# Kernel tuning notes

Measured on AMD Instinct MI355X. Metric: run time of the kernel, lower is better.

## Reference

```python
import jax, jax.numpy as jnp
import numpy as np

N = 256          # batch size
C = 100          # nb_classes
D = 512          # sz_embed
SCALE = 3.0
EPS = 1e-12      # F.normalize eps
M = N * (N - 1) // 2  # number of (i<j) candidate pairs


def l2norm(x):
    # matches F.normalize(p=2, dim=-1) with eps=1e-12
    return x / jnp.maximum(jnp.linalg.norm(x, axis=-1, keepdims=True), EPS)


def dist_block(A, B):
    # squared euclidean distance block of pairwise_distance(cat([A,B]))[0][:len(A), len(A):]
    # (off-diagonal block, so the eye-masking in the original is a no-op; negatives zeroed)
    d = (A * A).sum(-1, keepdims=True) + (B * B).sum(-1)[None, :] - 2.0 * (A @ B.T)
    return jnp.maximum(d, 0.0)


def setup_inputs() -> dict:
    key = jax.random.key(0)
    k1, k2, k3 = jax.random.split(key, 3)
    X = jax.random.normal(k1, (N, D), dtype=jnp.float32)
    proxies = jax.random.normal(k2, (C, D), dtype=jnp.float32) / 8.0
    T = jax.random.randint(k3, (N,), 0, C)
    indices = jnp.arange(N)  # unused by forward, kept for signature fidelity
    return {"X": X, "proxies": proxies, "T": T, "indices": indices}


def reference(X, proxies, T, indices):
    Pn = SCALE * l2norm(proxies)           # (C, D)
    Xn = SCALE * l2norm(X)                 # (N, D)
    IP = Xn @ Pn.T                         # (N, C) inner-product block

    # --- intercls_mixup (method=1, uncertainty-guided lambdas) ---
    # all i<j pairs; same-class pairs are masked out (original skips them in a Python loop)
    i1, i2 = jnp.triu_indices(N, k=1)      # (M,), (M,)
    diff = T[i1] != T[i2]                  # (M,) valid cross-class pairs
    c1, c2 = T[i1], T[i2]

    X1P1 = jnp.clip(IP[i1, c1], -1.0, 1.0)
    X1P2 = jnp.clip(IP[i1, c2], -1.0, 1.0)
    X2P1 = jnp.clip(IP[i2, c1], -1.0, 1.0)
    X2P2 = jnp.clip(IP[i2, c2], -1.0, 1.0)
    lam = jnp.clip((X2P2 - X2P1) / (X2P2 - X2P1 + X1P1 - X1P2), 0.3, 0.7)
    lam = jnp.where(diff, lam, 0.5)        # neutralize masked (same-class) pairs

    virt = lam[:, None] * Xn[i1] + (1.0 - lam[:, None]) * Xn[i2]  # (M, D)
    virt = l2norm(virt)

    # --- proxy-NCA loss over real + virtual samples ---
    Xall = jnp.concatenate([Xn, SCALE * virt], axis=0)            # (N+M, D)
    Dall = dist_block(Xall, Pn)                                   # (N+M, C)
    logsm = jax.nn.log_softmax(-Dall, axis=-1)

    loss_real = -logsm[jnp.arange(N), T]                          # one-hot targets
    lv = logsm[N:]                                                # (M, C)
    rows = jnp.arange(M)
    # virtual soft targets: lam*onehot(c1) + (1-lam)*onehot(c2)
    loss_virt = -(lam * lv[rows, c1] + (1.0 - lam) * lv[rows, c2])

    total = loss_real.sum() + jnp.sum(jnp.where(diff, loss_virt, 0.0))
    count = N + diff.sum()
    return total / count
```

## Files before the change

kernel.cpp:

```cpp
#include <hip/hip_runtime.h>
#include <hip/hip_bf16.h>
#include <math.h>

#define N_ 256
#define C_ 100
#define D_ 512
#define LOG2E 1.44269504088896f
#define XPST 102
#define PBROWB 64
#define PBSLAB 6464

#define OFF_PB    0
#define OFF_XPN   103424
#define OFF_TL    156056
#define OFF_HIST  157080
#define OFF_SPS   157480
#define OFF_RED   157928
#define OFF_S2    157960
#define LDS_TOTAL 157992

typedef __attribute__((ext_vector_type(8))) short short8;
typedef __attribute__((ext_vector_type(4))) float floatx4;

__device__ inline float waveReduceSum(float v) {
    #pragma unroll
    for (int off = 32; off > 0; off >>= 1) v += __shfl_xor(v, off, 64);
    return v;
}
__device__ inline float clip1(float x) { return fminf(fmaxf(x, -1.0f), 1.0f); }

__device__ inline short8 cvt8(float4 a, float4 b) {
    union { __hip_bfloat16 h[8]; short8 s; } u;
    u.h[0] = __float2bfloat16(a.x); u.h[1] = __float2bfloat16(a.y);
    u.h[2] = __float2bfloat16(a.z); u.h[3] = __float2bfloat16(a.w);
    u.h[4] = __float2bfloat16(b.x); u.h[5] = __float2bfloat16(b.y);
    u.h[6] = __float2bfloat16(b.z); u.h[7] = __float2bfloat16(b.w);
    return u.s;
}

__global__ __launch_bounds__(512)
void fused_kernel(const float* __restrict__ X, const float* __restrict__ P,
                  const int* __restrict__ T, float* __restrict__ out) {
    extern __shared__ char smem[];
    short* Pb   = (short*)(smem + OFF_PB);
    float* XPn  = (float*)(smem + OFF_XPN);
    int*   Tl   = (int*)(smem + OFF_TL);
    int*   hist = (int*)(smem + OFF_HIST);
    float* sps  = (float*)(smem + OFF_SPS);
    float* red  = (float*)(smem + OFF_RED);
    float* s2   = (float*)(smem + OFF_S2);

    int t = threadIdx.x;
    int w = t >> 6, lane = t & 63;
    int b = blockIdx.x;

    if (t < C_) hist[t] = 0;
    if (t < N_) Tl[t] = T[t];

    for (int j = 0; j < 13; ++j) {
        int ch = t + 512 * j;
        float s8 = 0.0f;
        if (ch < 6400) {
            int pr = ch >> 6, cl = ch & 63;
            const float4* pp = (const float4*)(P + (size_t)pr * D_ + cl * 8);
            float4 a = pp[0], c4 = pp[1];
            s8 = a.x*a.x + a.y*a.y + a.z*a.z + a.w*a.w
               + c4.x*c4.x + c4.y*c4.y + c4.z*c4.z + c4.w*c4.w;
            short8 v = cvt8(a, c4);
            *(short8*)((char*)Pb + (cl >> 2) * PBSLAB + pr * PBROWB + (cl & 3) * 16) = v;
        }
        float rs = waveReduceSum(s8);
        int pr0 = w + 8 * j;
        if (lane == 0 && pr0 < C_) sps[pr0] = 3.0f * rsqrtf(fmaxf(rs, 1e-24f));
    }
    if (t < 64) {
        const float4* xp = (const float4*)(X + (size_t)b * D_ + t * 8);
        short8 v = cvt8(xp[0], xp[1]);
        *(short8*)((char*)Pb + (t >> 2) * PBSLAB + 100 * PBROWB + (t & 3) * 16) = v;
    }
    float sxb;
    {
        const float4* xp = (const float4*)(X + (size_t)b * D_ + lane * 8);
        float4 a = xp[0], c4 = xp[1];
        float xb2 = a.x*a.x + a.y*a.y + a.z*a.z + a.w*a.w
                  + c4.x*c4.x + c4.y*c4.y + c4.z*c4.z + c4.w*c4.w;
        xb2 = waveReduceSum(xb2);
        sxb = 3.0f * rsqrtf(fmaxf(xb2, 1e-24f));
    }

    __syncthreads();

    if (t < N_) atomicAdd(&hist[Tl[t]], 1);

    int r = lane & 15, quad = lane >> 4;
    int boff[7];
    #pragma unroll
    for (int tn = 0; tn < 7; ++tn) {
        int cb = tn * 16 + r;
        if (cb > 100) cb = 0;
        boff[tn] = cb * PBROWB + quad * 16;
    }
    for (int rt = w; rt < 9; rt += 8) {
        int lr0 = rt * 16;
        int ra = (b + lr0 + r) & 255;
        const float* arow = X + (size_t)ra * D_;
        floatx4 acc[7];
        #pragma unroll
        for (int tn = 0; tn < 7; ++tn) acc[tn] = (floatx4){0.f, 0.f, 0.f, 0.f};
        float nrm = 0.0f;
        #pragma unroll 4
        for (int kc = 0; kc < D_; kc += 32) {
            const float4* ap = (const float4*)(arow + kc + quad * 8);
            float4 a0 = ap[0], a1 = ap[1];
            nrm += a0.x*a0.x + a0.y*a0.y + a0.z*a0.z + a0.w*a0.w
                 + a1.x*a1.x + a1.y*a1.y + a1.z*a1.z + a1.w*a1.w;
            short8 av = cvt8(a0, a1);
            const char* sl = (const char*)Pb + (kc >> 5) * PBSLAB;
            #pragma unroll
            for (int tn = 0; tn < 7; ++tn) {
                short8 bv = *(const short8*)(sl + boff[tn]);
                acc[tn] = __builtin_amdgcn_mfma_f32_16x16x32_bf16(av, bv, acc[tn], 0, 0, 0);
            }
        }
        nrm += __shfl_xor(nrm, 16, 64);
        nrm += __shfl_xor(nrm, 32, 64);
        float sxa = 3.0f * rsqrtf(fmaxf(nrm, 1e-24f));
        float sxr[4];
        #pragma unroll
        for (int i = 0; i < 4; ++i) sxr[i] = __shfl(sxa, quad * 4 + i, 64);
        #pragma unroll
        for (int tn = 0; tn < 7; ++tn) {
            int colw = tn * 16 + r;
            if (colw <= 100) {
                float cs = (colw < 100) ? sps[colw] : sxb;
                #pragma unroll
                for (int i = 0; i < 4; ++i) {
                    int lr = lr0 + quad * 4 + i;
                    if (lr <= 128) XPn[lr * XPST + colw] = acc[tn][i] * sxr[i] * cs;
                }
            }
        }
    }
    __syncthreads();

    float same = 0.0f;
    if (t < C_) { float n = (float)hist[t]; same = 0.5f * n * (n - 1.0f); }
    float rsame = waveReduceSum(same);
    if (lane == 0) s2[w] = rsame;

    int m = t >> 1, p = t & 1;
    bool diag = (m == 128);
    int d = m + 1;
    int lr2 = diag ? 0 : d;
    int i2 = diag ? b : ((b + d) & 255);
    bool isPair = (m < 127) || (m == 127 && b < 128);
    int t1 = Tl[b], t2 = Tl[i2];
    bool act = diag || (isPair && (t2 != t1));
    float contrib = 0.0f;
    if (__ballot(act)) {
        if (act) {
            const float* rowA = XPn;
            const float* rowB = XPn + lr2 * XPST;
            float ip11 = rowA[t1], ip12 = rowA[t2];
            float ip21 = rowB[t1], ip22 = rowB[t2];
            float X1P1 = clip1(ip11), X1P2 = clip1(ip12);
            float X2P1 = clip1(ip21), X2P2 = clip1(ip22);
            float num = X2P2 - X2P1;
            float den = num + X1P1 - X1P2;
            float lam = fminf(fmaxf(num / den, 0.3f), 0.7f);
            if (diag) lam = 1.0f;
            float oml = 1.0f - lam;
            float g = rowB[100];
            float wn2 = 9.0f * (lam * lam + oml * oml) + 2.0f * lam * oml * g;
            float ss2 = 6.0f * rsqrtf(fmaxf(wn2, 1e-24f));
            float la = ss2 * lam * LOG2E, lb = ss2 * oml * LOG2E;
            float sm0 = 0, sm1 = 0, sm2 = 0, sm3 = 0;
            #pragma unroll 4
            for (int k = 0; k < 13; ++k) {
                int c = 4 * p + 8 * k;
                if (c < C_) {
                    sm0 += exp2f(la * rowA[c]     + lb * rowB[c]);
                    sm1 += exp2f(la * rowA[c + 1] + lb * rowB[c + 1]);
                    sm2 += exp2f(la * rowA[c + 2] + lb * rowB[c + 2]);
                    sm3 += exp2f(la * rowA[c + 3] + lb * rowB[c + 3]);
                }
            }
            float sm = (sm0 + sm1) + (sm2 + sm3);
            sm += __shfl_xor(sm, 1, 64);
            if (p == 0) {
                float LSE = logf(sm);
                float ec1 = ss2 * (lam * ip11 + oml * ip21);
                float ec2 = ss2 * (lam * ip12 + oml * ip22);
                contrib = LSE - lam * ec1 - oml * ec2;
            }
        }
    }
    contrib = waveReduceSum(contrib);
    if (lane == 0) red[w] = contrib;
    __syncthreads();
    if (t == 0) {
        float bs = 0.0f, sc = 0.0f;
        #pragma unroll
        for (int k = 0; k < 8; ++k) { bs += red[k]; sc += s2[k]; }
        atomicAdd(out, bs / (32896.0f - sc));
    }
}

extern "C" void kernel_launch(void* const* d_in, const int* in_sizes, int n_in,
                              void* d_out, int out_size, void* d_ws, size_t ws_size,
                              hipStream_t stream) {
    const float* X = (const float*)d_in[0];
    const float* P = (const float*)d_in[1];
    const int*   T = (const int*)d_in[2];
    float* out = (float*)d_out;

    static bool init = false;
    if (!init) {
        hipFuncSetAttribute((const void*)fused_kernel,
                            hipFuncAttributeMaxDynamicSharedMemorySize, LDS_TOTAL);
        init = true;
    }
    fused_kernel<<<N_, 512, LDS_TOTAL, stream>>>(X, P, T, out);
}
```

Measured before the change: 83.69 us.

## Precompute bf16 slabs and row norms in a prep kernel, rebalance MFMA tiling

Adds a prep kernel that computes the L2 scale factors and converts X and the proxies to bf16 in a k-slab layout in workspace, done once instead of in each of the 256 blocks. The fused kernel now copies the pre-converted proxy slabs into LDS and reads X rows as bf16 straight from global. The MFMA work is redistributed so each wave does 2 row tiles by 4 or 3 column tiles, sharing each B load across two A tiles. The softmax stage is reorganized to use 4 threads per pair with float4 LDS reads. This costs a second kernel launch and a workspace round-trip, and the leftover row 128 gets extra serial work on one wave group.

```diff
diff --git a/kernel.cpp b/kernel.cpp
--- a/kernel.cpp
+++ b/kernel.cpp
@@ -6,18 +6,23 @@
 #define C_ 100
 #define D_ 512
 #define LOG2E 1.44269504088896f
-#define XPST 102
-#define PBROWB 64
-#define PBSLAB 6464
-
+
+#define WS_XF   0
+#define WS_PF   262144
+#define WS_SXS  364544
+#define WS_SPS  365568
+
+#define PB_SLAB   6656
 #define OFF_PB    0
-#define OFF_XPN   103424
-#define OFF_TL    156056
-#define OFF_HIST  157080
-#define OFF_SPS   157480
-#define OFF_RED   157928
-#define OFF_S2    157960
-#define LDS_TOTAL 157992
+#define XPST      104
+#define OFF_XPN   106496
+#define OFF_SXS   160160
+#define OFF_SPS   161184
+#define OFF_TL    161600
+#define OFF_HIST  162624
+#define OFF_RED   163024
+#define OFF_S2    163056
+#define LDS_TOTAL 163088
 
 typedef __attribute__((ext_vector_type(8))) short short8;
 typedef __attribute__((ext_vector_type(4))) float floatx4;
@@ -38,105 +43,147 @@
     return u.s;
 }
 
+__global__ __launch_bounds__(256)
+void prep_kernel(const float* __restrict__ X, const float* __restrict__ P,
+                 char* __restrict__ ws) {
+    int w = blockIdx.x * 4 + (threadIdx.x >> 6);
+    if (w >= 356) return;
+    int lane = threadIdx.x & 63;
+    bool isX = (w < N_);
+    int rrow = isX ? w : (w - N_);
+    const float* src = isX ? (X + (size_t)w * D_) : (P + (size_t)(w - N_) * D_);
+    const float4* sp4 = (const float4*)src + lane * 2;
+    float4 a = sp4[0], b2 = sp4[1];
+    float s8 = a.x*a.x + a.y*a.y + a.z*a.z + a.w*a.w
+             + b2.x*b2.x + b2.y*b2.y + b2.z*b2.z + b2.w*b2.w;
+    float tot = waveReduceSum(s8);
+    float sc = 3.0f * rsqrtf(fmaxf(tot, 1e-24f));
+    if (lane == 0) {
+        if (isX) ((float*)(ws + WS_SXS))[rrow] = sc;
+        else     ((float*)(ws + WS_SPS))[rrow] = sc;
+    }
+    short8 v = cvt8(a, b2);
+    char* base = ws + (isX ? WS_XF : WS_PF);
+    int rowsN = isX ? 256 : 100;
+    *(short8*)(base + ((size_t)(lane >> 2) * rowsN + rrow) * 64 + (lane & 3) * 16) = v;
+}
+
 __global__ __launch_bounds__(512)
-void fused_kernel(const float* __restrict__ X, const float* __restrict__ P,
-                  const int* __restrict__ T, float* __restrict__ out) {
+void fused_kernel(const char* __restrict__ ws, const int* __restrict__ T,
+                  float* __restrict__ out) {
     extern __shared__ char smem[];
-    short* Pb   = (short*)(smem + OFF_PB);
-    float* XPn  = (float*)(smem + OFF_XPN);
-    int*   Tl   = (int*)(smem + OFF_TL);
-    int*   hist = (int*)(smem + OFF_HIST);
-    float* sps  = (float*)(smem + OFF_SPS);
-    float* red  = (float*)(smem + OFF_RED);
-    float* s2   = (float*)(smem + OFF_S2);
+    char*  PbC   = smem + OFF_PB;
+    float* XPn   = (float*)(smem + OFF_XPN);
+    float* sxs_l = (float*)(smem + OFF_SXS);
+    float* sps_l = (float*)(smem + OFF_SPS);
+    int*   Tl    = (int*)(smem + OFF_TL);
+    int*   hist  = (int*)(smem + OFF_HIST);
+    float* red   = (float*)(smem + OFF_RED);
+    float* s2    = (float*)(smem + OFF_S2);
 
     int t = threadIdx.x;
     int w = t >> 6, lane = t & 63;
     int b = blockIdx.x;
-
-    if (t < C_) hist[t] = 0;
-    if (t < N_) Tl[t] = T[t];
-
-    for (int j = 0; j < 13; ++j) {
-        int ch = t + 512 * j;
-        float s8 = 0.0f;
-        if (ch < 6400) {
-            int pr = ch >> 6, cl = ch & 63;
-            const float4* pp = (const float4*)(P + (size_t)pr * D_ + cl * 8);
-            float4 a = pp[0], c4 = pp[1];
-            s8 = a.x*a.x + a.y*a.y + a.z*a.z + a.w*a.w
-               + c4.x*c4.x + c4.y*c4.y + c4.z*c4.z + c4.w*c4.w;
-            short8 v = cvt8(a, c4);
-            *(short8*)((char*)Pb + (cl >> 2) * PBSLAB + pr * PBROWB + (cl & 3) * 16) = v;
-        }
-        float rs = waveReduceSum(s8);
-        int pr0 = w + 8 * j;
-        if (lane == 0 && pr0 < C_) sps[pr0] = 3.0f * rsqrtf(fmaxf(rs, 1e-24f));
+    const char* Xfc = ws + WS_XF;
+    const char* Pfc = ws + WS_PF;
+
+    #pragma unroll
+    for (int it = 0; it < 13; ++it) {
+        int id = t + 512 * it;
+        if (id < 6400) {
+            int slab = id / 400;
+            int within = id - slab * 400;
+            *(short8*)(PbC + slab * PB_SLAB + within * 16) =
+                *(const short8*)(Pfc + (size_t)slab * 6400 + within * 16);
+        }
     }
     if (t < 64) {
-        const float4* xp = (const float4*)(X + (size_t)b * D_ + t * 8);
-        short8 v = cvt8(xp[0], xp[1]);
-        *(short8*)((char*)Pb + (t >> 2) * PBSLAB + 100 * PBROWB + (t & 3) * 16) = v;
-    }
-    float sxb;
-    {
-        const float4* xp = (const float4*)(X + (size_t)b * D_ + lane * 8);
-        float4 a = xp[0], c4 = xp[1];
-        float xb2 = a.x*a.x + a.y*a.y + a.z*a.z + a.w*a.w
-                  + c4.x*c4.x + c4.y*c4.y + c4.z*c4.z + c4.w*c4.w;
-        xb2 = waveReduceSum(xb2);
-        sxb = 3.0f * rsqrtf(fmaxf(xb2, 1e-24f));
-    }
-
+        *(short8*)(PbC + (t >> 2) * PB_SLAB + 6400 + (t & 3) * 16) =
+            *(const short8*)(Xfc + ((size_t)(t >> 2) * 256 + b) * 64 + (t & 3) * 16);
+    }
+    if (t < N_) { sxs_l[t] = ((const float*)(ws + WS_SXS))[t]; Tl[t] = T[t]; }
+    if (t < C_) { sps_l[t] = ((const float*)(ws + WS_SPS))[t]; hist[t] = 0; }
     __syncthreads();
-
     if (t < N_) atomicAdd(&hist[Tl[t]], 1);
 
     int r = lane & 15, quad = lane >> 4;
-    int boff[7];
-    #pragma unroll
-    for (int tn = 0; tn < 7; ++tn) {
-        int cb = tn * 16 + r;
-        if (cb > 100) cb = 0;
-        boff[tn] = cb * PBROWB + quad * 16;
-    }
-    for (int rt = w; rt < 9; rt += 8) {
-        int lr0 = rt * 16;
-        int ra = (b + lr0 + r) & 255;
-        const float* arow = X + (size_t)ra * D_;
-        floatx4 acc[7];
-        #pragma unroll
-        for (int tn = 0; tn < 7; ++tn) acc[tn] = (floatx4){0.f, 0.f, 0.f, 0.f};
-        float nrm = 0.0f;
+    int rh = w >> 1, ch = w & 1;
+    int ra0 = (b + rh * 16 + r) & 255;
+    int ra1 = (b + (rh + 4) * 16 + r) & 255;
+    int aoff0 = ra0 * 64 + quad * 16;
+    int aoff1 = ra1 * 64 + quad * 16;
+    int ct0 = ch ? 4 : 0, nct = ch ? 3 : 4;
+    int boff[4];
+    #pragma unroll
+    for (int j = 0; j < 4; ++j)
+        boff[j] = ((ct0 + j) * 16 + r) * 64 + quad * 16;
+
+    floatx4 acc[2][4];
+    #pragma unroll
+    for (int i = 0; i < 2; ++i)
+        #pragma unroll
+        for (int j = 0; j < 4; ++j) acc[i][j] = (floatx4){0.f, 0.f, 0.f, 0.f};
+
+    #pragma unroll 4
+    for (int ks = 0; ks < 16; ++ks) {
+        const char* ab = Xfc + (size_t)ks * 16384;
+        short8 a0 = *(const short8*)(ab + aoff0);
+        short8 a1 = *(const short8*)(ab + aoff1);
+        const char* bb = PbC + ks * PB_SLAB;
+        #pragma unroll
+        for (int j = 0; j < 4; ++j) {
+            if (j < nct) {
+                short8 bv = *(const short8*)(bb + boff[j]);
+                acc[0][j] = __builtin_amdgcn_mfma_f32_16x16x32_bf16(a0, bv, acc[0][j], 0, 0, 0);
+                acc[1][j] = __builtin_amdgcn_mfma_f32_16x16x32_bf16(a1, bv, acc[1][j], 0, 0, 0);
+            }
+        }
+    }
+    #pragma unroll
+    for (int rtid = 0; rtid < 2; ++rtid) {
+        int rt = rtid ? (rh + 4) : rh;
+        #pragma unroll
+        for (int j = 0; j < 4; ++j) {
+            if (j < nct) {
+                int c = (ct0 + j) * 16 + r;
+                if (c <= 100) {
+                    float cs = (c < 100) ? sps_l[c] : sxs_l[b];
+                    #pragma unroll
+                    for (int i = 0; i < 4; ++i) {
+                        int lr = rt * 16 + quad * 4 + i;
+                        XPn[lr * XPST + c] = acc[rtid][j][i] * sxs_l[(b + lr) & 255] * cs;
+                    }
+                }
+            }
+        }
+    }
+    if (b < 128 && rh == 3) {
+        int ra8 = (b + 128 + r) & 255;
+        int aoff8 = ra8 * 64 + quad * 16;
+        floatx4 acc8[4];
+        #pragma unroll
+        for (int j = 0; j < 4; ++j) acc8[j] = (floatx4){0.f, 0.f, 0.f, 0.f};
         #pragma unroll 4
-        for (int kc = 0; kc < D_; kc += 32) {
-            const float4* ap = (const float4*)(arow + kc + quad * 8);
-            float4 a0 = ap[0], a1 = ap[1];
-            nrm += a0.x*a0.x + a0.y*a0.y + a0.z*a0.z + a0.w*a0.w
-                 + a1.x*a1.x + a1.y*a1.y + a1.z*a1.z + a1.w*a1.w;
-            short8 av = cvt8(a0, a1);
-            const char* sl = (const char*)Pb + (kc >> 5) * PBSLAB;
+        for (int ks = 0; ks < 16; ++ks) {
+            short8 a8 = *(const short8*)(Xfc + (size_t)ks * 16384 + aoff8);
+            const char* bb = PbC + ks * PB_SLAB;
             #pragma unroll
-            for (int tn = 0; tn < 7; ++tn) {
-                short8 bv = *(const short8*)(sl + boff[tn]);
-                acc[tn] = __builtin_amdgcn_mfma_f32_16x16x32_bf16(av, bv, acc[tn], 0, 0, 0);
-            }
-        }
-        nrm += __shfl_xor(nrm, 16, 64);
-        nrm += __shfl_xor(nrm, 32, 64);
-        float sxa = 3.0f * rsqrtf(fmaxf(nrm, 1e-24f));
-        float sxr[4];
-        #pragma unroll
-        for (int i = 0; i < 4; ++i) sxr[i] = __shfl(sxa, quad * 4 + i, 64);
-        #pragma unroll
-        for (int tn = 0; tn < 7; ++tn) {
-            int colw = tn * 16 + r;
-            if (colw <= 100) {
-                float cs = (colw < 100) ? sps[colw] : sxb;
-                #pragma unroll
-                for (int i = 0; i < 4; ++i) {
-                    int lr = lr0 + quad * 4 + i;
-                    if (lr <= 128) XPn[lr * XPST + colw] = acc[tn][i] * sxr[i] * cs;
+            for (int j = 0; j < 4; ++j) {
+                if (j < nct) {
+                    short8 bv = *(const short8*)(bb + boff[j]);
+                    acc8[j] = __builtin_amdgcn_mfma_f32_16x16x32_bf16(a8, bv, acc8[j], 0, 0, 0);
+                }
+            }
+        }
+        if (quad == 0) {
+            #pragma unroll
+            for (int j = 0; j < 4; ++j) {
+                if (j < nct) {
+                    int c = (ct0 + j) * 16 + r;
+                    if (c <= 100) {
+                        float cs = (c < 100) ? sps_l[c] : sxs_l[b];
+                        XPn[128 * XPST + c] = acc8[j][0] * sxs_l[(b + 128) & 255] * cs;
+                    }
                 }
             }
         }
@@ -148,51 +195,51 @@
     float rsame = waveReduceSum(same);
     if (lane == 0) s2[w] = rsame;
 
-    int m = t >> 1, p = t & 1;
-    bool diag = (m == 128);
-    int d = m + 1;
-    int lr2 = diag ? 0 : d;
-    int i2 = diag ? b : ((b + d) & 255);
-    bool isPair = (m < 127) || (m == 127 && b < 128);
-    int t1 = Tl[b], t2 = Tl[i2];
-    bool act = diag || (isPair && (t2 != t1));
+    int m = t >> 2, q = t & 3;
+    int t1 = Tl[b];
     float contrib = 0.0f;
-    if (__ballot(act)) {
-        if (act) {
-            const float* rowA = XPn;
-            const float* rowB = XPn + lr2 * XPST;
-            float ip11 = rowA[t1], ip12 = rowA[t2];
-            float ip21 = rowB[t1], ip22 = rowB[t2];
-            float X1P1 = clip1(ip11), X1P2 = clip1(ip12);
-            float X2P1 = clip1(ip21), X2P2 = clip1(ip22);
-            float num = X2P2 - X2P1;
-            float den = num + X1P1 - X1P2;
-            float lam = fminf(fmaxf(num / den, 0.3f), 0.7f);
-            if (diag) lam = 1.0f;
-            float oml = 1.0f - lam;
-            float g = rowB[100];
-            float wn2 = 9.0f * (lam * lam + oml * oml) + 2.0f * lam * oml * g;
-            float ss2 = 6.0f * rsqrtf(fmaxf(wn2, 1e-24f));
-            float la = ss2 * lam * LOG2E, lb = ss2 * oml * LOG2E;
-            float sm0 = 0, sm1 = 0, sm2 = 0, sm3 = 0;
-            #pragma unroll 4
-            for (int k = 0; k < 13; ++k) {
-                int c = 4 * p + 8 * k;
-                if (c < C_) {
-                    sm0 += exp2f(la * rowA[c]     + lb * rowB[c]);
-                    sm1 += exp2f(la * rowA[c + 1] + lb * rowB[c + 1]);
-                    sm2 += exp2f(la * rowA[c + 2] + lb * rowB[c + 2]);
-                    sm3 += exp2f(la * rowA[c + 3] + lb * rowB[c + 3]);
-                }
-            }
-            float sm = (sm0 + sm1) + (sm2 + sm3);
-            sm += __shfl_xor(sm, 1, 64);
-            if (p == 0) {
-                float LSE = logf(sm);
-                float ec1 = ss2 * (lam * ip11 + oml * ip21);
-                float ec2 = ss2 * (lam * ip12 + oml * ip22);
-                contrib = LSE - lam * ec1 - oml * ec2;
-            }
+    int nit = (m == 127) ? ((b < 128) ? 2 : 1) : 1;
+    for (int it = 0; it < nit; ++it) {
+        bool isdiag = (m == 127) && (it == 0);
+        int dd = isdiag ? 0 : ((m == 127) ? 128 : (m + 1));
+        int i2 = (b + dd) & 255;
+        int t2 = Tl[i2];
+        if (!(isdiag || (t2 != t1))) continue;
+        const float* rowA = XPn;
+        const float* rowB = XPn + dd * XPST;
+        float ip11 = rowA[t1], ip12 = rowA[t2];
+        float ip21 = rowB[t1], ip22 = rowB[t2];
+        float X1P1 = clip1(ip11), X1P2 = clip1(ip12);
+        float X2P1 = clip1(ip21), X2P2 = clip1(ip22);
+        float num = X2P2 - X2P1;
+        float den = num + X1P1 - X1P2;
+        float lam = fminf(fmaxf(num / den, 0.3f), 0.7f);
+        if (isdiag) lam = 1.0f;
+        float oml = 1.0f - lam;
+        float g = rowB[100];
+        float wn2 = 9.0f * (lam * lam + oml * oml) + 2.0f * lam * oml * g;
+        float ss2 = 6.0f * rsqrtf(fmaxf(wn2, 1e-24f));
+        float la = ss2 * lam * LOG2E, lb = ss2 * oml * LOG2E;
+        float sm = 0.0f;
+        #pragma unroll
+        for (int k = 0; k < 7; ++k) {
+            int c = q * 4 + 16 * k;
+            if (c < C_) {
+                float4 a1 = *(const float4*)(rowA + c);
+                float4 a2 = *(const float4*)(rowB + c);
+                sm += exp2f(la * a1.x + lb * a2.x);
+                sm += exp2f(la * a1.y + lb * a2.y);
+                sm += exp2f(la * a1.z + lb * a2.z);
+                sm += exp2f(la * a1.w + lb * a2.w);
+            }
+        }
+        sm += __shfl_xor(sm, 1, 64);
+        sm += __shfl_xor(sm, 2, 64);
+        if (q == 0) {
+            float LSE = logf(sm);
+            float ec1 = ss2 * (lam * ip11 + oml * ip21);
+            float ec2 = ss2 * (lam * ip12 + oml * ip22);
+            contrib += LSE - lam * ec1 - oml * ec2;
         }
     }
     contrib = waveReduceSum(contrib);
@@ -212,6 +259,7 @@
     const float* X = (const float*)d_in[0];
     const float* P = (const float*)d_in[1];
     const int*   T = (const int*)d_in[2];
+    char* ws = (char*)d_ws;
     float* out = (float*)d_out;
 
     static bool init = false;
@@ -220,5 +268,6 @@
                             hipFuncAttributeMaxDynamicSharedMemorySize, LDS_TOTAL);
         init = true;
     }
-    fused_kernel<<<N_, 512, LDS_TOTAL, stream>>>(X, P, T, out);
-}
+    prep_kernel<<<89, 256, 0, stream>>>(X, P, ws);
+    fused_kernel<<<N_, 512, LDS_TOTAL, stream>>>(ws, T, out);
+}
```

Result: faster. 76.61 us (-8.5%).
